# Kernel optimization log

Hardware: AMD Instinct MI355X
Metric: run time of the kernel (lower is better)

The kernel has to match this reference:

```python
import jax, jax.numpy as jnp
import numpy as np

LN2 = float(np.log(2.0))
CUTOFF_L = 0.5


def _ssp(x):
    # shifted softplus: log(0.5*exp(x) + 0.5)
    return jax.nn.softplus(x) - LN2


def _pair_idx(n):
    # ordered pairs arranged [n, n-1]: for each i, all j != i
    idx = np.arange(n)
    j = np.stack([np.concatenate([idx[:k], idx[k + 1:]]) for k in range(n)])  # [n, n-1]
    i = np.broadcast_to(idx[:, None], j.shape)
    return jnp.asarray(i), jnp.asarray(j)


def _mlp3(x, w1, b1, w2, b2, w3, b3):
    h = _ssp(x @ w1 + b1)
    h = _ssp(h @ w2 + b2)
    return h @ w3 + b3


def _backflow_cutoff(r, L=CUTOFF_L):
    r = r / L
    return jnp.where(r < L, r ** 2 * (6.0 - 8.0 * r + 3.0 * r ** 2), jnp.ones((), r.dtype))


def setup_inputs() -> dict:
    key = jax.random.key(0)
    ks = jax.random.split(key, 12)
    B, N, D, K = 512, 32, 256, 8
    dims_e = [D, 40, 6, 1]
    dims_n = [D, 81, 25, 8]

    def lin(k, fi, fo):
        return jax.random.normal(k, (fi, fo), jnp.float32) / np.sqrt(fi)

    inp = {
        'rs': jax.random.normal(ks[0], (B, N, 3), jnp.float32),
        'xs': jax.random.normal(ks[1], (B, N, D), jnp.float32),
        'coords': jax.random.normal(ks[2], (K, 3), jnp.float32) * 2.0,
        'ew1': lin(ks[3], dims_e[0], dims_e[1]), 'eb1': jnp.zeros((dims_e[1],), jnp.float32),
        'ew2': lin(ks[4], dims_e[1], dims_e[2]), 'eb2': jnp.zeros((dims_e[2],), jnp.float32),
        'ew3': lin(ks[5], dims_e[2], dims_e[3]), 'eb3': jnp.zeros((dims_e[3],), jnp.float32),
        'nw1': lin(ks[6], dims_n[0], dims_n[1]), 'nb1': jnp.zeros((dims_n[1],), jnp.float32),
        'nw2': lin(ks[7], dims_n[1], dims_n[2]), 'nb2': jnp.zeros((dims_n[2],), jnp.float32),
        'nw3': lin(ks[8], dims_n[2], dims_n[3]), 'nb3': jnp.zeros((dims_n[3],), jnp.float32),
    }
    return inp


def reference(rs, xs, coords, ew1, eb1, ew2, eb2, ew3, eb3,
              nw1, nb1, nw2, nb2, nw3, nb3):
    n_elec = rs.shape[-2]
    i, j = _pair_idx(n_elec)  # [n, n-1] static index arrays

    # electron-electron backflow
    diffs_elec = rs[..., i, :] - rs[..., j, :]                    # [B, n, n-1, 3]
    pair_feat = xs[..., i, :] * xs[..., j, :]                     # [B, n, n-1, D]
    w_pair = _mlp3(pair_feat, ew1, eb1, ew2, eb2, ew3, eb3)       # [B, n, n-1, 1]
    bf_elec = (w_pair * diffs_elec).sum(axis=-2)                  # [B, n, 3]

    # electron-nucleus backflow
    diffs_nuc = rs[..., :, None, :] - coords                      # [B, n, K, 3]
    w_nuc = _mlp3(xs, nw1, nb1, nw2, nb2, nw3, nb3)               # [B, n, K]
    bf_nuc = (w_nuc[..., None] * diffs_nuc).sum(axis=-2)          # [B, n, 3]

    dist_nuc = jnp.linalg.norm(diffs_nuc, axis=-1)                # [B, n, K]
    cutoff = _backflow_cutoff(dist_nuc).prod(axis=-1)             # [B, n]

    return rs + 1e-4 * cutoff[..., None] * (bf_elec + bf_nuc)
```

## Files before the change

### kernel.cpp

```cpp
#include <hip/hip_runtime.h>
#include <stdint.h>


static constexpr int B_ = 512, N_ = 32, D_ = 256, K_ = 8;
static constexpr int E1 = 40, E2 = 6;
static constexpr int N1 = 81, N2 = 25, N3 = 8;
static constexpr int HEP = 96;
static constexpr float LN2f = 0.69314718055994530942f;
static constexpr float L2Ef = 1.44269504088896340736f;

typedef float    f32x4 __attribute__((ext_vector_type(4)));
typedef _Float16 f16x8 __attribute__((ext_vector_type(8)));
typedef _Float16 f16x4 __attribute__((ext_vector_type(4)));

#define MFMA32(A, B, C) __builtin_amdgcn_mfma_f32_16x16x32_f16((A), (B), (C), 0, 0, 0)
#if __has_builtin(__builtin_amdgcn_mfma_f32_16x16x16_f16)
#define MFMA16(A, B, C) __builtin_amdgcn_mfma_f32_16x16x16_f16((A), (B), (C), 0, 0, 0)
#else
#define MFMA16(A, B, C) __builtin_amdgcn_mfma_f32_16x16x16f16((A), (B), (C), 0, 0, 0)
#endif

__device__ __forceinline__ float ssp2(float t) {
    float e = __builtin_amdgcn_exp2f(t);
    return __builtin_amdgcn_logf(fmaf(e, 0.5f, 0.5f));
}

__device__ __forceinline__ void lds_dma16(void* lds, const void* g) {
    __builtin_amdgcn_global_load_lds(
        (const __attribute__((address_space(1))) unsigned int*)(uintptr_t)g,
        (__attribute__((address_space(3))) unsigned int*)(uintptr_t)lds,
        16, 0, 0);
}

__global__ __launch_bounds__(256) void k_prep(
    const float* __restrict__ ew1, const float* __restrict__ nw1,
    const float* __restrict__ nw2, _Float16* __restrict__ wsp)
{
    const int g = blockIdx.x * 256 + threadIdx.x;
    _Float16* ew1T = wsp;
    _Float16* nw1T = wsp + 48 * 256;
    _Float16* nw2T = wsp + 48 * 256 + 96 * 256;

    if (g < 1536) {
        const int n = g >> 5, kb = g & 31;
        f16x8 v;
        #pragma unroll
        for (int d = 0; d < 8; ++d) {
            const int k = kb * 8 + d;
            v[d] = (_Float16)((n < E1) ? ew1[k * E1 + n] * L2Ef : 0.f);
        }
        *(f16x8*)&ew1T[n * 256 + ((kb ^ (n & 7)) << 3)] = v;
    } else if (g < 4608) {
        const int q = g - 1536;
        const int n = q >> 5, kb = q & 31;
        f16x8 v;
        #pragma unroll
        for (int d = 0; d < 8; ++d) {
            const int k = kb * 8 + d;
            v[d] = (_Float16)((n < N1) ? nw1[k * N1 + n] * L2Ef : 0.f);
        }
        *(f16x8*)&nw1T[n * 256 + kb * 8] = v;
    } else if (g < 4992) {
        const int q = g - 4608;
        const int n = q / 12, kb = q - n * 12;
        f16x8 v;
        #pragma unroll
        for (int d = 0; d < 8; ++d) {
            const int kk = kb * 8 + d;
            v[d] = (_Float16)((n < N2 && kk < N1) ? nw2[kk * N2 + n] : 0.f);
        }
        *(f16x8*)&nw2T[n * 96 + kb * 8] = v;
    }
}

__global__ __launch_bounds__(512, 2) void k_fused(
    const float* __restrict__ rs, const float* __restrict__ xs,
    const float* __restrict__ coords,
    const float* __restrict__ eb1, const float* __restrict__ ew2,
    const float* __restrict__ eb2, const float* __restrict__ ew3,
    const float* __restrict__ eb3, const float* __restrict__ nb1,
    const float* __restrict__ nb2, const float* __restrict__ nb3,
    const float* __restrict__ nw3, const _Float16* __restrict__ wsp,
    float* __restrict__ out)
{
    __shared__ alignas(16) _Float16 xs_h[N_ * 256];
    __shared__ alignas(16) _Float16 ew1T_s[48 * 256];
    __shared__ alignas(16) _Float16 h1e[16 * HEP];
    __shared__ alignas(16) float    h2e[16 * 26];
    __shared__ alignas(16) float    eb1_s[48];
    __shared__ alignas(16) float    b2_s[16];
    __shared__ float rs_s[96], nw3_s[200], nb2_s[32], nb3_s[8], co_s[24];
    __shared__ float bfn_s[48], cut_s[16], bfe_s[48];

    const int bid = blockIdx.x;
    const int b = bid >> 1, rbase = (bid & 1) << 4;
    const int t = threadIdx.x;
    const int wv = t >> 6, l = t & 63, quad = l >> 4, c = l & 15;

    const _Float16* ew1T_g = wsp;
    const _Float16* nw1T_g = wsp + 48 * 256;
    const _Float16* nw2T_g = wsp + 48 * 256 + 96 * 256;

    {
        const char* g = (const char*)ew1T_g;
        char* d = (char*)ew1T_s;
        const int wb = wv * 1024;
        #pragma unroll
        for (int r = 0; r < 3; ++r)
            lds_dma16(d + r * 8192 + wb, g + r * 8192 + wb + (l << 4));
    }
    {
        const float4* src = (const float4*)(xs + (size_t)b * N_ * D_);
        #pragma unroll
        for (int u = 0; u < 2; ++u) {
            const int idx = t + 512 * u;
            const int row = idx >> 5, kb = idx & 31;
            float4 v0 = src[idx << 1];
            float4 v1 = src[(idx << 1) + 1];
            union { _Float16 h[8]; uint4 q; } pk;
            pk.h[0] = (_Float16)v0.x; pk.h[1] = (_Float16)v0.y;
            pk.h[2] = (_Float16)v0.z; pk.h[3] = (_Float16)v0.w;
            pk.h[4] = (_Float16)v1.x; pk.h[5] = (_Float16)v1.y;
            pk.h[6] = (_Float16)v1.z; pk.h[7] = (_Float16)v1.w;
            *(uint4*)&xs_h[row * 256 + ((kb ^ (row & 7)) << 3)] = pk.q;
        }
    }
    if (t < 96)  rs_s[t] = rs[b * 96 + t];
    if (t < 200) nw3_s[t] = nw3[t] * LN2f;
    if (t < N2)  nb2_s[t] = nb2[t] * L2Ef;
    if (t < N3)  nb3_s[t] = nb3[t];
    if (t < 24)  co_s[t] = coords[t];
    if (t < 48)  eb1_s[t] = (t < E1) ? eb1[t] * L2Ef : 0.f;
    if (t < 16)  b2_s[t] = (t < E2) ? eb2[t] * L2Ef : 0.f;
    if (t < 384) ((uint64_t*)h1e)[t] = 0ull;

    f16x4 b2fT[3];
    #pragma unroll
    for (int Nt = 0; Nt < 3; ++Nt) {
        f16x4 p;
        #pragma unroll
        for (int r = 0; r < 4; ++r) {
            const int n = Nt * 16 + quad * 4 + r;
            p[r] = (_Float16)((n < E1 && c < E2) ? ew2[n * E2 + c] : 0.f);
        }
        b2fT[Nt] = p;
    }
    float w3q[4];
    #pragma unroll
    for (int r = 0; r < 4; ++r) {
        const int m = quad * 4 + r;
        w3q[r] = (m < E2) ? ew3[m] * LN2f : 0.f;
    }
    const float eb3v = eb3[0];

    __syncthreads();

    if (wv < 6) {
        const int n_col = wv * 16 + c;
        const float nb1v = (n_col < N1) ? nb1[n_col] * L2Ef : 0.f;
        const _Float16* bg = nw1T_g + n_col * 256 + quad * 8;
        f32x4 acc1 = (f32x4){0.f, 0.f, 0.f, 0.f};
        f16x8 Bp = *(const f16x8*)bg;
        #pragma unroll
        for (int Kt = 0; Kt < 8; ++Kt) {
            f16x8 Bf = Bp;
            if (Kt < 7) Bp = *(const f16x8*)(bg + (Kt + 1) * 32);
            f16x8 A = *(const f16x8*)&xs_h[(rbase + c) * 256 +
                                           (((Kt * 4 + quad) ^ (c & 7)) << 3)];
            acc1 = MFMA32(A, Bf, acc1);
        }
        if (n_col < N1) {
            #pragma unroll
            for (int r2 = 0; r2 < 4; ++r2)
                h1e[(quad * 4 + r2) * HEP + n_col] = (_Float16)ssp2(acc1[r2] + nb1v);
        }
    }

    {
        const int i0 = rbase + wv, i1 = i0 + 8;
        f32x4 acc[2][2][3];
        #pragma unroll
        for (int Nt = 0; Nt < 3; ++Nt) {
            f32x4 bias = *(const f32x4*)&eb1_s[Nt * 16 + quad * 4];
            acc[0][0][Nt] = bias; acc[0][1][Nt] = bias;
            acc[1][0][Nt] = bias; acc[1][1][Nt] = bias;
        }
        #pragma unroll
        for (int Kt = 0; Kt < 8; ++Kt) {
            const int kb = Kt * 4 + quad;
            const int sj = (kb ^ (c & 7)) << 3;
            const int si = (kb ^ wv) << 3;
            f16x8 iv0 = *(const f16x8*)&xs_h[i0 * 256 + si];
            f16x8 iv1 = *(const f16x8*)&xs_h[i1 * 256 + si];
            f16x8 jv0 = *(const f16x8*)&xs_h[c * 256 + sj];
            f16x8 jv1 = *(const f16x8*)&xs_h[(16 + c) * 256 + sj];
            f16x8 P00 = iv0 * jv0;
            f16x8 P01 = iv0 * jv1;
            f16x8 P10 = iv1 * jv0;
            f16x8 P11 = iv1 * jv1;
            #pragma unroll
            for (int Nt = 0; Nt < 3; ++Nt) {
                f16x8 b1 = *(const f16x8*)&ew1T_s[(Nt * 16 + c) * 256 + sj];
                acc[0][0][Nt] = MFMA32(b1, P00, acc[0][0][Nt]);
                acc[0][1][Nt] = MFMA32(b1, P01, acc[0][1][Nt]);
                acc[1][0][Nt] = MFMA32(b1, P10, acc[1][0][Nt]);
                acc[1][1][Nt] = MFMA32(b1, P11, acc[1][1][Nt]);
            }
        }
        const f32x4 b2i = *(const f32x4*)&b2_s[quad * 4];
        #pragma unroll
        for (int ih = 0; ih < 2; ++ih) {
            const int lr = wv + ih * 8, i = rbase + lr;
            const float rix = rs_s[i * 3 + 0], riy = rs_s[i * 3 + 1],
                        riz = rs_s[i * 3 + 2];
            float cxi = 0.f, cyi = 0.f, czi = 0.f;
            #pragma unroll
            for (int h = 0; h < 2; ++h) {
                f32x4 acc2 = b2i;
                #pragma unroll
                for (int Nt = 0; Nt < 3; ++Nt) {
                    f16x4 bh_;
                    #pragma unroll
                    for (int r2 = 0; r2 < 4; ++r2)
                        bh_[r2] = (_Float16)ssp2(acc[ih][h][Nt][r2]);
                    acc2 = MFMA16(b2fT[Nt], bh_, acc2);
                }
                float wsum = 0.f;
                #pragma unroll
                for (int r2 = 0; r2 < 4; ++r2)
                    wsum = fmaf(w3q[r2], ssp2(acc2[r2]), wsum);
                wsum += __shfl_xor(wsum, 16);
                wsum += __shfl_xor(wsum, 32);
                const float wj = wsum + eb3v;
                const int j = c + 16 * h;
                cxi = fmaf(wj, rix - rs_s[j * 3 + 0], cxi);
                cyi = fmaf(wj, riy - rs_s[j * 3 + 1], cyi);
                czi = fmaf(wj, riz - rs_s[j * 3 + 2], czi);
            }
            #pragma unroll
            for (int m2 = 1; m2 < 16; m2 <<= 1) {
                cxi += __shfl_xor(cxi, m2);
                cyi += __shfl_xor(cyi, m2);
                czi += __shfl_xor(czi, m2);
            }
            if (l == 0) {
                bfe_s[lr * 3 + 0] = cxi;
                bfe_s[lr * 3 + 1] = cyi;
                bfe_s[lr * 3 + 2] = czi;
            }
        }
    }
    __syncthreads();

    if (wv < 2) {
        const int n = wv * 16 + c;
        const _Float16* bg2 = nw2T_g + n * 96 + quad * 8;
        f32x4 acc2 = (f32x4){0.f, 0.f, 0.f, 0.f};
        #pragma unroll
        for (int Kt2 = 0; Kt2 < 3; ++Kt2) {
            f16x8 A  = *(const f16x8*)&h1e[c * HEP + Kt2 * 32 + quad * 8];
            f16x8 Bf = *(const f16x8*)(bg2 + Kt2 * 32);
            acc2 = MFMA32(A, Bf, acc2);
        }
        if (n < N2) {
            #pragma unroll
            for (int r2 = 0; r2 < 4; ++r2)
                h2e[(quad * 4 + r2) * 26 + n] = ssp2(acc2[r2] + nb2_s[n]);
        }
    }
    __syncthreads();

    if (t < 128) {
        const int r = t >> 3, s = t & 7;
        const int gi = rbase + r;
        float w = nb3_s[s];
        const int rb26 = r * 26;
        #pragma unroll
        for (int kk = 0; kk < N2; ++kk)
            w = fmaf(h2e[rb26 + kk], nw3_s[kk * N3 + s], w);
        const float dx = rs_s[gi * 3 + 0] - co_s[s * 3 + 0];
        const float dy = rs_s[gi * 3 + 1] - co_s[s * 3 + 1];
        const float dz = rs_s[gi * 3 + 2] - co_s[s * 3 + 2];
        float cx = w * dx, cy = w * dy, cz = w * dz;
        #pragma unroll
        for (int m2 = 1; m2 < 8; m2 <<= 1) {
            cx += __shfl_xor(cx, m2);
            cy += __shfl_xor(cy, m2);
            cz += __shfl_xor(cz, m2);
        }
        const float rr  = sqrtf(dx * dx + dy * dy + dz * dz);
        const float xsc = 2.f * rr;
        float cf = (xsc < 0.5f) ? xsc * xsc * (6.f - 8.f * xsc + 3.f * xsc * xsc) : 1.f;
        #pragma unroll
        for (int m2 = 1; m2 < 8; m2 <<= 1) cf *= __shfl_xor(cf, m2);
        if (s == 0) {
            bfn_s[r * 3 + 0] = cx;
            bfn_s[r * 3 + 1] = cy;
            bfn_s[r * 3 + 2] = cz;
            cut_s[r] = cf;
        }
    }
    __syncthreads();

    if (t < 48) {
        const int r = t / 3;
        out[(size_t)b * (N_ * 3) + rbase * 3 + t] =
            rs_s[rbase * 3 + t] + 1e-4f * cut_s[r] * (bfe_s[t] + bfn_s[t]);
    }
}

extern "C" void kernel_launch(void* const* d_in, const int* in_sizes, int n_in,
                              void* d_out, int out_size, void* d_ws, size_t ws_size,
                              hipStream_t stream)
{
    const float* rs     = (const float*)d_in[0];
    const float* xs     = (const float*)d_in[1];
    const float* coords = (const float*)d_in[2];
    const float* ew1    = (const float*)d_in[3];
    const float* eb1    = (const float*)d_in[4];
    const float* ew2    = (const float*)d_in[5];
    const float* eb2    = (const float*)d_in[6];
    const float* ew3    = (const float*)d_in[7];
    const float* eb3    = (const float*)d_in[8];
    const float* nw1    = (const float*)d_in[9];
    const float* nb1    = (const float*)d_in[10];
    const float* nw2    = (const float*)d_in[11];
    const float* nb2    = (const float*)d_in[12];
    const float* nw3    = (const float*)d_in[13];
    const float* nb3    = (const float*)d_in[14];

    _Float16* wsp = (_Float16*)d_ws;

    k_prep<<<20, 256, 0, stream>>>(ew1, nw1, nw2, wsp);
    k_fused<<<B_ * 2, 512, 0, stream>>>(rs, xs, coords, eb1, ew2, eb2, ew3, eb3,
                                        nb1, nb2, nb3, nw3, wsp, (float*)d_out);
}
```

Before: 124.5 us.

## Shrink LDS footprint to raise k_fused occupancy to four blocks per CU

Trims the padded ew1 transpose from 48 to 40 rows, drops several small shared arrays in favour of registers or direct global reads, and aliases h2e, bfn_s and cut_s onto buffers that are dead by then. The launch bound goes from 2 to 4 blocks per CU so more blocks can be resident and hide latency. The third N-tile of the edge MLP now reads a clamped row and zeroes its B fragment for the missing columns. The risks are register pressure under the tighter bound and more scalar global loads in the tail.

```diff
diff --git a/kernel.cpp b/kernel.cpp
--- a/kernel.cpp
+++ b/kernel.cpp
@@ -38,20 +38,20 @@
 {
     const int g = blockIdx.x * 256 + threadIdx.x;
     _Float16* ew1T = wsp;
-    _Float16* nw1T = wsp + 48 * 256;
-    _Float16* nw2T = wsp + 48 * 256 + 96 * 256;
-
-    if (g < 1536) {
+    _Float16* nw1T = wsp + 40 * 256;
+    _Float16* nw2T = wsp + 40 * 256 + 96 * 256;
+
+    if (g < 1280) {
         const int n = g >> 5, kb = g & 31;
         f16x8 v;
         #pragma unroll
         for (int d = 0; d < 8; ++d) {
             const int k = kb * 8 + d;
-            v[d] = (_Float16)((n < E1) ? ew1[k * E1 + n] * L2Ef : 0.f);
+            v[d] = (_Float16)(ew1[k * E1 + n] * L2Ef);
         }
         *(f16x8*)&ew1T[n * 256 + ((kb ^ (n & 7)) << 3)] = v;
-    } else if (g < 4608) {
-        const int q = g - 1536;
+    } else if (g < 4352) {
+        const int q = g - 1280;
         const int n = q >> 5, kb = q & 31;
         f16x8 v;
         #pragma unroll
@@ -60,8 +60,8 @@
             v[d] = (_Float16)((n < N1) ? nw1[k * N1 + n] * L2Ef : 0.f);
         }
         *(f16x8*)&nw1T[n * 256 + kb * 8] = v;
-    } else if (g < 4992) {
-        const int q = g - 4608;
+    } else if (g < 4736) {
+        const int q = g - 4352;
         const int n = q / 12, kb = q - n * 12;
         f16x8 v;
         #pragma unroll
@@ -73,7 +73,7 @@
     }
 }
 
-__global__ __launch_bounds__(512, 2) void k_fused(
+__global__ __launch_bounds__(512, 4) void k_fused(
     const float* __restrict__ rs, const float* __restrict__ xs,
     const float* __restrict__ coords,
     const float* __restrict__ eb1, const float* __restrict__ ew2,
@@ -84,13 +84,13 @@
     float* __restrict__ out)
 {
     __shared__ alignas(16) _Float16 xs_h[N_ * 256];
-    __shared__ alignas(16) _Float16 ew1T_s[48 * 256];
+    __shared__ alignas(16) _Float16 ew1T_s[40 * 256];
     __shared__ alignas(16) _Float16 h1e[16 * HEP];
-    __shared__ alignas(16) float    h2e[16 * 26];
-    __shared__ alignas(16) float    eb1_s[48];
-    __shared__ alignas(16) float    b2_s[16];
-    __shared__ float rs_s[96], nw3_s[200], nb2_s[32], nb3_s[8], co_s[24];
-    __shared__ float bfn_s[48], cut_s[16], bfe_s[48];
+    __shared__ alignas(16) float    rs_s[96];
+    __shared__ alignas(16) float    bfe_s[48];
+    float* h2e   = (float*)xs_h;
+    float* bfn_s = (float*)h1e;
+    float* cut_s = bfn_s + 48;
 
     const int bid = blockIdx.x;
     const int b = bid >> 1, rbase = (bid & 1) << 4;
@@ -98,16 +98,17 @@
     const int wv = t >> 6, l = t & 63, quad = l >> 4, c = l & 15;
 
     const _Float16* ew1T_g = wsp;
-    const _Float16* nw1T_g = wsp + 48 * 256;
-    const _Float16* nw2T_g = wsp + 48 * 256 + 96 * 256;
+    const _Float16* nw1T_g = wsp + 40 * 256;
+    const _Float16* nw2T_g = wsp + 40 * 256 + 96 * 256;
 
     {
         const char* g = (const char*)ew1T_g;
         char* d = (char*)ew1T_s;
         const int wb = wv * 1024;
-        #pragma unroll
-        for (int r = 0; r < 3; ++r)
-            lds_dma16(d + r * 8192 + wb, g + r * 8192 + wb + (l << 4));
+        lds_dma16(d + wb,        g + wb        + (l << 4));
+        lds_dma16(d + 8192 + wb, g + 8192 + wb + (l << 4));
+        if (wv < 4)
+            lds_dma16(d + 16384 + wb, g + 16384 + wb + (l << 4));
     }
     {
         const float4* src = (const float4*)(xs + (size_t)b * N_ * D_);
@@ -126,12 +127,6 @@
         }
     }
     if (t < 96)  rs_s[t] = rs[b * 96 + t];
-    if (t < 200) nw3_s[t] = nw3[t] * LN2f;
-    if (t < N2)  nb2_s[t] = nb2[t] * L2Ef;
-    if (t < N3)  nb3_s[t] = nb3[t];
-    if (t < 24)  co_s[t] = coords[t];
-    if (t < 48)  eb1_s[t] = (t < E1) ? eb1[t] * L2Ef : 0.f;
-    if (t < 16)  b2_s[t] = (t < E2) ? eb2[t] * L2Ef : 0.f;
     if (t < 384) ((uint64_t*)h1e)[t] = 0ull;
 
     f16x4 b2fT[3];
@@ -152,6 +147,24 @@
         w3q[r] = (m < E2) ? ew3[m] * LN2f : 0.f;
     }
     const float eb3v = eb3[0];
+    f32x4 b2i;
+    #pragma unroll
+    for (int r = 0; r < 4; ++r) {
+        const int m = quad * 4 + r;
+        b2i[r] = (m < E2) ? eb2[m] * L2Ef : 0.f;
+    }
+    f32x4 bias[3];
+    #pragma unroll
+    for (int Nt = 0; Nt < 3; ++Nt) {
+        const int n0 = Nt * 16 + quad * 4;
+        if (n0 < E1) {
+            f32x4 v = *(const f32x4*)&eb1[n0];
+            #pragma unroll
+            for (int r = 0; r < 4; ++r) bias[Nt][r] = v[r] * L2Ef;
+        } else {
+            bias[Nt] = (f32x4){0.f, 0.f, 0.f, 0.f};
+        }
+    }
 
     __syncthreads();
 
@@ -178,12 +191,13 @@
 
     {
         const int i0 = rbase + wv, i1 = i0 + 8;
+        const bool okN2 = (c < 8);
+        const int rowN2 = okN2 ? (32 + c) : 32;
         f32x4 acc[2][2][3];
         #pragma unroll
         for (int Nt = 0; Nt < 3; ++Nt) {
-            f32x4 bias = *(const f32x4*)&eb1_s[Nt * 16 + quad * 4];
-            acc[0][0][Nt] = bias; acc[0][1][Nt] = bias;
-            acc[1][0][Nt] = bias; acc[1][1][Nt] = bias;
+            acc[0][0][Nt] = bias[Nt]; acc[0][1][Nt] = bias[Nt];
+            acc[1][0][Nt] = bias[Nt]; acc[1][1][Nt] = bias[Nt];
         }
         #pragma unroll
         for (int Kt = 0; Kt < 8; ++Kt) {
@@ -198,16 +212,23 @@
             f16x8 P01 = iv0 * jv1;
             f16x8 P10 = iv1 * jv0;
             f16x8 P11 = iv1 * jv1;
-            #pragma unroll
-            for (int Nt = 0; Nt < 3; ++Nt) {
-                f16x8 b1 = *(const f16x8*)&ew1T_s[(Nt * 16 + c) * 256 + sj];
-                acc[0][0][Nt] = MFMA32(b1, P00, acc[0][0][Nt]);
-                acc[0][1][Nt] = MFMA32(b1, P01, acc[0][1][Nt]);
-                acc[1][0][Nt] = MFMA32(b1, P10, acc[1][0][Nt]);
-                acc[1][1][Nt] = MFMA32(b1, P11, acc[1][1][Nt]);
-            }
-        }
-        const f32x4 b2i = *(const f32x4*)&b2_s[quad * 4];
+            f16x8 b1a = *(const f16x8*)&ew1T_s[c * 256 + sj];
+            f16x8 b1b = *(const f16x8*)&ew1T_s[(16 + c) * 256 + sj];
+            f16x8 b1c = *(const f16x8*)&ew1T_s[rowN2 * 256 + sj];
+            if (!okN2) b1c = (f16x8)(_Float16)0.f;
+            acc[0][0][0] = MFMA32(b1a, P00, acc[0][0][0]);
+            acc[0][1][0] = MFMA32(b1a, P01, acc[0][1][0]);
+            acc[1][0][0] = MFMA32(b1a, P10, acc[1][0][0]);
+            acc[1][1][0] = MFMA32(b1a, P11, acc[1][1][0]);
+            acc[0][0][1] = MFMA32(b1b, P00, acc[0][0][1]);
+            acc[0][1][1] = MFMA32(b1b, P01, acc[0][1][1]);
+            acc[1][0][1] = MFMA32(b1b, P10, acc[1][0][1]);
+            acc[1][1][1] = MFMA32(b1b, P11, acc[1][1][1]);
+            acc[0][0][2] = MFMA32(b1c, P00, acc[0][0][2]);
+            acc[0][1][2] = MFMA32(b1c, P01, acc[0][1][2]);
+            acc[1][0][2] = MFMA32(b1c, P10, acc[1][0][2]);
+            acc[1][1][2] = MFMA32(b1c, P11, acc[1][1][2]);
+        }
         #pragma unroll
         for (int ih = 0; ih < 2; ++ih) {
             const int lr = wv + ih * 8, i = rbase + lr;
@@ -254,6 +275,7 @@
 
     if (wv < 2) {
         const int n = wv * 16 + c;
+        const float nb2v = (n < N2) ? nb2[n] * L2Ef : 0.f;
         const _Float16* bg2 = nw2T_g + n * 96 + quad * 8;
         f32x4 acc2 = (f32x4){0.f, 0.f, 0.f, 0.f};
         #pragma unroll
@@ -265,7 +287,7 @@
         if (n < N2) {
             #pragma unroll
             for (int r2 = 0; r2 < 4; ++r2)
-                h2e[(quad * 4 + r2) * 26 + n] = ssp2(acc2[r2] + nb2_s[n]);
+                h2e[(quad * 4 + r2) * 26 + n] = ssp2(acc2[r2] + nb2v) * LN2f;
         }
     }
     __syncthreads();
@@ -273,14 +295,14 @@
     if (t < 128) {
         const int r = t >> 3, s = t & 7;
         const int gi = rbase + r;
-        float w = nb3_s[s];
+        float w = nb3[s];
         const int rb26 = r * 26;
         #pragma unroll
         for (int kk = 0; kk < N2; ++kk)
-            w = fmaf(h2e[rb26 + kk], nw3_s[kk * N3 + s], w);
-        const float dx = rs_s[gi * 3 + 0] - co_s[s * 3 + 0];
-        const float dy = rs_s[gi * 3 + 1] - co_s[s * 3 + 1];
-        const float dz = rs_s[gi * 3 + 2] - co_s[s * 3 + 2];
+            w = fmaf(h2e[rb26 + kk], nw3[kk * N3 + s], w);
+        const float dx = rs_s[gi * 3 + 0] - coords[s * 3 + 0];
+        const float dy = rs_s[gi * 3 + 1] - coords[s * 3 + 1];
+        const float dz = rs_s[gi * 3 + 2] - coords[s * 3 + 2];
         float cx = w * dx, cy = w * dy, cz = w * dz;
         #pragma unroll
         for (int m2 = 1; m2 < 8; m2 <<= 1) {
```

Measured after the change: 126.0 us. Within noise of the previous version (+1.2%).
